# Optimization experiments

Hardware: AMD Instinct MI355X
Metric: run time of the kernel (lower is better)

## Reference

```python
import jax, jax.numpy as jnp
import numpy as np

B, S, D_IN, D_OUT = 4, 2048, 2048, 2048


def setup_inputs() -> dict:
    key = jax.random.key(0)
    k1, k2, k3, k4 = jax.random.split(key, 4)
    x = jax.random.normal(k1, (B, S, D_IN), dtype=jnp.float32)
    scale = 1.0 / np.sqrt(D_IN)
    Wq = jax.random.normal(k2, (D_IN, D_OUT), dtype=jnp.float32) * scale
    Wk = jax.random.normal(k3, (D_IN, D_OUT), dtype=jnp.float32) * scale
    Wv = jax.random.normal(k4, (D_IN, D_OUT), dtype=jnp.float32) * scale
    return {"x": x, "Wq": Wq, "Wk": Wk, "Wv": Wv}


def reference(x, Wq, Wk, Wv):
    # x: [B,S,D_in]; Wq/Wk/Wv: [D_in,D_out]
    q = x @ Wq  # [B,S,D_out]
    k = x @ Wk
    v = x @ Wv
    d_out = q.shape[-1]
    inv_sqrt_d = jnp.asarray(1.0 / np.sqrt(d_out), dtype=x.dtype)
    scores = jnp.einsum('bqd,bkd->bqk', q, k) * inv_sqrt_d  # [B,S,S]
    n = scores.shape[-1]
    causal = jnp.tril(jnp.ones((n, n), dtype=bool))  # True where attending allowed
    scores = jnp.where(causal[None, :, :], scores, jnp.asarray(-jnp.inf, scores.dtype))
    attn = jax.nn.softmax(scores, axis=-1)  # dropout p=0.0 -> identity
    return jnp.einsum('bqk,bkd->bqd', attn, v)  # [B,S,D_out]
```

## Files before the change

### kernel.cpp

```cpp
#include <hip/hip_runtime.h>
#include <cmath>

typedef __bf16 bfx8 __attribute__((ext_vector_type(8)));
typedef float f32x4 __attribute__((ext_vector_type(4)));
typedef unsigned short u16x8 __attribute__((ext_vector_type(8)));

static constexpr int BB = 4, SS = 2048, DD = 2048;

__device__ __forceinline__ unsigned short f2bf(float f) {
  unsigned u = __builtin_bit_cast(unsigned, f);
  u += 0x7fffu + ((u >> 16) & 1u);
  return (unsigned short)(u >> 16);
}

__device__ __forceinline__ void gload_lds16(const void* g, void* l) {
  __builtin_amdgcn_global_load_lds(
      (__attribute__((address_space(1))) unsigned int*)(g),
      (__attribute__((address_space(3))) unsigned int*)(l),
      16, 0, 0);
}

template <int CMODE>
__global__ __launch_bounds__(256) void gemm_bt(
    const unsigned short* __restrict__ A, const unsigned short* __restrict__ B,
    void* __restrict__ Cv, int N, int K,
    long long sA, long long sB, long long sC, float scale)
{
  const int bx = blockIdx.x, by = blockIdx.y, bz = blockIdx.z;
  if (CMODE == 1 && bx > by) return;
  const int t = threadIdx.x;
  const int wave = t >> 6, lane = t & 63;
  const int fr = lane & 15, fk = lane >> 4;
  const int m0 = by << 7, n0 = bx << 7;

  __shared__ __align__(16) char lds[32768];

  const unsigned short* Ab = A + (size_t)bz * sA;
  const unsigned short* Bb = B + (size_t)bz * sB;

  const unsigned short* aSrc[4];
  const unsigned short* bSrc[4];
  int ldsOff[4];
#pragma unroll
  for (int i = 0; i < 4; ++i) {
    int c = i * 256 + t;
    int row = c >> 3;
    int scb = ((c & 7) << 4) ^ ((row & 7) << 4);
    aSrc[i] = Ab + (size_t)(m0 + row) * K + (scb >> 1);
    bSrc[i] = Bb + (size_t)(n0 + row) * K + (scb >> 1);
    ldsOff[i] = i * 4096 + wave * 1024;
  }

  int ktiles = K >> 6;
  if (CMODE == 2) ktiles = min(ktiles, (by + 1) * 2);

  f32x4 acc[4][4] = {};
  const int wr = (wave >> 1) << 6;
  const int wc = (wave & 1) << 6;
  const int sx = (fr & 7) << 4;

  for (int kt = 0; kt < ktiles; ++kt) {
    __syncthreads();
#pragma unroll
    for (int i = 0; i < 4; ++i) {
      gload_lds16(aSrc[i], &lds[ldsOff[i]]);
      gload_lds16(bSrc[i], &lds[16384 + ldsOff[i]]);
      aSrc[i] += 64;
      bSrc[i] += 64;
    }
    __syncthreads();
#pragma unroll
    for (int kk = 0; kk < 2; ++kk) {
      bfx8 af[4], bfv[4];
#pragma unroll
      for (int mi = 0; mi < 4; ++mi) {
        int ar = wr + mi * 16 + fr;
        af[mi] = *(const bfx8*)&lds[ar * 128 + ((kk * 64 + fk * 16) ^ sx)];
      }
#pragma unroll
      for (int ni = 0; ni < 4; ++ni) {
        int br = wc + ni * 16 + fr;
        bfv[ni] = *(const bfx8*)&lds[16384 + br * 128 + ((kk * 64 + fk * 16) ^ sx)];
      }
#pragma unroll
      for (int mi = 0; mi < 4; ++mi)
#pragma unroll
        for (int ni = 0; ni < 4; ++ni)
          acc[mi][ni] = __builtin_amdgcn_mfma_f32_16x16x32_bf16(
              af[mi], bfv[ni], acc[mi][ni], 0, 0, 0);
    }
  }

#pragma unroll
  for (int mi = 0; mi < 4; ++mi) {
#pragma unroll
    for (int ni = 0; ni < 4; ++ni) {
      int r0 = m0 + wr + mi * 16 + fk * 4;
      int cn = n0 + wc + ni * 16 + fr;
      if (CMODE == 0) {
        unsigned short* C = (unsigned short*)Cv + (size_t)bz * sC;
#pragma unroll
        for (int j = 0; j < 4; ++j)
          C[(size_t)(r0 + j) * N + cn] = f2bf(acc[mi][ni][j]);
      } else if (CMODE == 1 || CMODE == 2) {
        float* C = (float*)Cv + (size_t)bz * sC;
#pragma unroll
        for (int j = 0; j < 4; ++j)
          C[(size_t)(r0 + j) * N + cn] = acc[mi][ni][j] * scale;
      } else {
        unsigned short* VT = (unsigned short*)Cv;
        int b = r0 >> 11, s0v = r0 & 2047;
        ushort4 pk;
        pk.x = f2bf(acc[mi][ni][0]);
        pk.y = f2bf(acc[mi][ni][1]);
        pk.z = f2bf(acc[mi][ni][2]);
        pk.w = f2bf(acc[mi][ni][3]);
        *(ushort4*)&VT[(size_t)b * DD * SS + (size_t)cn * SS + s0v] = pk;
      }
    }
  }
}

__global__ __launch_bounds__(256) void cvt_x_kernel(
    const float* __restrict__ x, unsigned short* __restrict__ xb)
{
  size_t i = ((size_t)blockIdx.x * 256 + threadIdx.x) * 8;
  float4 a = *(const float4*)(x + i);
  float4 b = *(const float4*)(x + i + 4);
  u16x8 o = {f2bf(a.x), f2bf(a.y), f2bf(a.z), f2bf(a.w),
             f2bf(b.x), f2bf(b.y), f2bf(b.z), f2bf(b.w)};
  *(u16x8*)(xb + i) = o;
}

__global__ __launch_bounds__(256) void cvt_wT_kernel(
    const float* __restrict__ Wq, const float* __restrict__ Wk,
    const float* __restrict__ Wv, unsigned short* __restrict__ Wt)
{
  const float* W = blockIdx.z == 0 ? Wq : (blockIdx.z == 1 ? Wk : Wv);
  unsigned short* out = Wt + (size_t)blockIdx.z * DD * DD;
  __shared__ unsigned short tile[64][65];
  int k0 = blockIdx.y * 64, n0 = blockIdx.x * 64;
#pragma unroll
  for (int i = 0; i < 16; ++i) {
    int idx = threadIdx.x + i * 256;
    int r = idx >> 6, c = idx & 63;
    tile[r][c] = f2bf(W[(size_t)(k0 + r) * DD + n0 + c]);
  }
  __syncthreads();
#pragma unroll
  for (int i = 0; i < 16; ++i) {
    int idx = threadIdx.x + i * 256;
    int r = idx >> 6, c = idx & 63;
    out[(size_t)(n0 + r) * DD + k0 + c] = tile[c][r];
  }
}

__global__ __launch_bounds__(256) void softmax_causal(
    const float* __restrict__ Sc, unsigned short* __restrict__ P)
{
  const int i = blockIdx.x, b = blockIdx.y, t = threadIdx.x;
  const float* srow = Sc + ((size_t)b * SS + i) * SS;
  unsigned short* prow = P + ((size_t)b * SS + i) * SS;
  const int j0 = t * 8;
  float4 v0 = *(const float4*)(srow + j0);
  float4 v1 = *(const float4*)(srow + j0 + 4);
  float s[8] = {v0.x, v0.y, v0.z, v0.w, v1.x, v1.y, v1.z, v1.w};
  float mx = -INFINITY;
#pragma unroll
  for (int e = 0; e < 8; ++e) {
    if (j0 + e > i) s[e] = -INFINITY;
    mx = fmaxf(mx, s[e]);
  }
#pragma unroll
  for (int off = 32; off; off >>= 1) mx = fmaxf(mx, __shfl_xor(mx, off));
  __shared__ float red[8];
  if ((t & 63) == 0) red[t >> 6] = mx;
  __syncthreads();
  mx = fmaxf(fmaxf(red[0], red[1]), fmaxf(red[2], red[3]));
  float e8[8];
  float sm = 0.f;
#pragma unroll
  for (int e = 0; e < 8; ++e) {
    e8[e] = (j0 + e <= i) ? __expf(s[e] - mx) : 0.f;
    sm += e8[e];
  }
#pragma unroll
  for (int off = 32; off; off >>= 1) sm += __shfl_xor(sm, off);
  if ((t & 63) == 0) red[4 + (t >> 6)] = sm;
  __syncthreads();
  float inv = 1.0f / (red[4] + red[5] + red[6] + red[7]);
  u16x8 o;
#pragma unroll
  for (int e = 0; e < 8; ++e) o[e] = f2bf(e8[e] * inv);
  *(u16x8*)(prow + j0) = o;
}

extern "C" void kernel_launch(void* const* d_in, const int* in_sizes, int n_in,
                              void* d_out, int out_size, void* d_ws, size_t ws_size,
                              hipStream_t stream)
{
  const float* x  = (const float*)d_in[0];
  const float* Wq = (const float*)d_in[1];
  const float* Wk = (const float*)d_in[2];
  const float* Wv = (const float*)d_in[3];
  float* out = (float*)d_out;

  const size_t MR = (size_t)BB * SS;
  unsigned short* xb = (unsigned short*)d_ws;
  unsigned short* Wt = xb + MR * DD;
  unsigned short* qk = Wt + 3ull * DD * DD;
  unsigned short* vt = qk + 2ull * MR * DD;
  float* sc = (float*)(vt + (size_t)BB * DD * SS);
  unsigned short* P = (unsigned short*)(sc + (size_t)BB * SS * SS);

  cvt_x_kernel<<<dim3(8192), 256, 0, stream>>>(x, xb);
  cvt_wT_kernel<<<dim3(32, 32, 3), 256, 0, stream>>>(Wq, Wk, Wv, Wt);

  gemm_bt<0><<<dim3(16, 64, 2), 256, 0, stream>>>(
      xb, Wt, qk, DD, DD, 0, (long long)DD * DD, (long long)(MR * DD), 1.f);
  gemm_bt<3><<<dim3(16, 64, 1), 256, 0, stream>>>(
      xb, Wt + 2ull * DD * DD, vt, DD, DD, 0, 0, 0, 1.f);

  const float iscale = 1.0f / sqrtf((float)DD);
  gemm_bt<1><<<dim3(16, 16, 4), 256, 0, stream>>>(
      qk, qk + MR * DD, sc, SS, DD,
      (long long)(SS * (size_t)DD), (long long)(SS * (size_t)DD),
      (long long)(SS * (size_t)SS), iscale);

  softmax_causal<<<dim3(SS, BB), 256, 0, stream>>>(sc, P);

  gemm_bt<2><<<dim3(16, 16, 4), 256, 0, stream>>>(
      P, vt, out, DD, SS,
      (long long)(SS * (size_t)SS), (long long)(DD * (size_t)SS),
      (long long)(SS * (size_t)DD), 1.f);
}
```

Measured before the change: 556.9 us.

## Use 256x256 double-buffered GEMM tiles with 8 waves and compute V^T via swapped operands

The bf16 GEMM kernel moves from 128x128 tiles with 4 waves to 256x256 tiles with 8 waves. It uses a double-buffered 128KB LDS pipeline: the next K-tile's loads are issued partway through the current tile's MFMA work, and MFMA sections are raised in priority with setprio. The special transposed-store path for V is removed, and V^T is produced by a regular GEMM of Wv^T against x, one batch per z slice. This aims to raise data reuse per LDS load and hide global-load latency. In exchange, the large LDS footprint limits occupancy to one block per CU, and the causal GEMMs now skip work at a coarser tile granularity.

```diff
diff --git a/kernel.cpp b/kernel.cpp
--- a/kernel.cpp
+++ b/kernel.cpp
@@ -21,7 +21,7 @@
 }
 
 template <int CMODE>
-__global__ __launch_bounds__(256) void gemm_bt(
+__global__ __launch_bounds__(512, 2) void gemm_bt(
     const unsigned short* __restrict__ A, const unsigned short* __restrict__ B,
     void* __restrict__ Cv, int N, int K,
     long long sA, long long sB, long long sC, float scale)
@@ -31,91 +31,110 @@
   const int t = threadIdx.x;
   const int wave = t >> 6, lane = t & 63;
   const int fr = lane & 15, fk = lane >> 4;
-  const int m0 = by << 7, n0 = bx << 7;
-
-  __shared__ __align__(16) char lds[32768];
+  const int wr = wave >> 2;
+  const int wc = wave & 3;
+  const int m0 = by << 8, n0 = bx << 8;
+
+  __shared__ __align__(16) char lds[131072];
 
   const unsigned short* Ab = A + (size_t)bz * sA;
   const unsigned short* Bb = B + (size_t)bz * sB;
 
-  const unsigned short* aSrc[4];
-  const unsigned short* bSrc[4];
-  int ldsOff[4];
-#pragma unroll
-  for (int i = 0; i < 4; ++i) {
-    int c = i * 256 + t;
+  const unsigned short* aS[4];
+  const unsigned short* bS[4];
+  int lOff[4];
+#pragma unroll
+  for (int j = 0; j < 4; ++j) {
+    int c = ((j >> 1) << 10) + ((j & 1) << 9) + t;
     int row = c >> 3;
-    int scb = ((c & 7) << 4) ^ ((row & 7) << 4);
-    aSrc[i] = Ab + (size_t)(m0 + row) * K + (scb >> 1);
-    bSrc[i] = Bb + (size_t)(n0 + row) * K + (scb >> 1);
-    ldsOff[i] = i * 4096 + wave * 1024;
+    int sb = ((c & 7) << 4) ^ ((row & 7) << 4);
+    aS[j] = Ab + (size_t)(m0 + row) * K + (sb >> 1);
+    bS[j] = Bb + (size_t)(n0 + row) * K + (sb >> 1);
+    lOff[j] = ((j >> 1) << 14) + ((j & 1) << 13) + (wave << 10);
   }
 
   int ktiles = K >> 6;
-  if (CMODE == 2) ktiles = min(ktiles, (by + 1) * 2);
-
-  f32x4 acc[4][4] = {};
-  const int wr = (wave >> 1) << 6;
-  const int wc = (wave & 1) << 6;
+  if (CMODE == 2) ktiles = min(ktiles, (by + 1) * 4);
+
+  f32x4 acc[8][4] = {};
   const int sx = (fr & 7) << 4;
+  const int aRowB = wr << 7;
+  const int bRowB = wc << 6;
+
+#pragma unroll
+  for (int j = 0; j < 4; ++j) { gload_lds16(aS[j], lds + lOff[j]); aS[j] += 64; }
+#pragma unroll
+  for (int j = 0; j < 4; ++j) { gload_lds16(bS[j], lds + 32768 + lOff[j]); bS[j] += 64; }
+  asm volatile("s_waitcnt vmcnt(0)" ::: "memory");
+  __builtin_amdgcn_s_barrier();
 
   for (int kt = 0; kt < ktiles; ++kt) {
-    __syncthreads();
-#pragma unroll
-    for (int i = 0; i < 4; ++i) {
-      gload_lds16(aSrc[i], &lds[ldsOff[i]]);
-      gload_lds16(bSrc[i], &lds[16384 + ldsOff[i]]);
-      aSrc[i] += 64;
-      bSrc[i] += 64;
+    const int cb = (kt & 1) << 16;
+    const int nb = cb ^ 65536;
+    const bool pf = (kt + 1 < ktiles);
+    const char* la = lds + cb;
+    const char* lb = lds + cb + 32768;
+#pragma unroll
+    for (int q = 0; q < 4; ++q) {
+      const int mb = (q & 1) << 2;
+      const int nbf = (q >> 1) << 1;
+      bfx8 af[4][2], bv[2][2];
+#pragma unroll
+      for (int mi = 0; mi < 4; ++mi) {
+        int row = aRowB + ((mb + mi) << 4) + fr;
+#pragma unroll
+        for (int kk = 0; kk < 2; ++kk)
+          af[mi][kk] = *(const bfx8*)(la + row * 128 + (((kk << 6) + (fk << 4)) ^ sx));
+      }
+#pragma unroll
+      for (int ni = 0; ni < 2; ++ni) {
+        int row = bRowB + ((nbf + ni) << 4) + fr;
+#pragma unroll
+        for (int kk = 0; kk < 2; ++kk)
+          bv[ni][kk] = *(const bfx8*)(lb + row * 128 + (((kk << 6) + (fk << 4)) ^ sx));
+      }
+      if (q == 0 && pf) {
+#pragma unroll
+        for (int j = 0; j < 4; ++j) { gload_lds16(aS[j], lds + nb + lOff[j]); aS[j] += 64; }
+      }
+      if (q == 1 && pf) {
+#pragma unroll
+        for (int j = 0; j < 4; ++j) { gload_lds16(bS[j], lds + nb + 32768 + lOff[j]); bS[j] += 64; }
+      }
+      __builtin_amdgcn_s_barrier();
+      asm volatile("s_waitcnt lgkmcnt(0)" ::: "memory");
+      __builtin_amdgcn_sched_barrier(0);
+      __builtin_amdgcn_s_setprio(1);
+#pragma unroll
+      for (int kk = 0; kk < 2; ++kk)
+#pragma unroll
+        for (int mi = 0; mi < 4; ++mi)
+#pragma unroll
+          for (int ni = 0; ni < 2; ++ni)
+            acc[mb + mi][nbf + ni] = __builtin_amdgcn_mfma_f32_16x16x32_bf16(
+                af[mi][kk], bv[ni][kk], acc[mb + mi][nbf + ni], 0, 0, 0);
+      __builtin_amdgcn_s_setprio(0);
+      if (q == 3) asm volatile("s_waitcnt vmcnt(0)" ::: "memory");
+      __builtin_amdgcn_s_barrier();
     }
-    __syncthreads();
-#pragma unroll
-    for (int kk = 0; kk < 2; ++kk) {
-      bfx8 af[4], bfv[4];
-#pragma unroll
-      for (int mi = 0; mi < 4; ++mi) {
-        int ar = wr + mi * 16 + fr;
-        af[mi] = *(const bfx8*)&lds[ar * 128 + ((kk * 64 + fk * 16) ^ sx)];
-      }
-#pragma unroll
-      for (int ni = 0; ni < 4; ++ni) {
-        int br = wc + ni * 16 + fr;
-        bfv[ni] = *(const bfx8*)&lds[16384 + br * 128 + ((kk * 64 + fk * 16) ^ sx)];
-      }
-#pragma unroll
-      for (int mi = 0; mi < 4; ++mi)
-#pragma unroll
-        for (int ni = 0; ni < 4; ++ni)
-          acc[mi][ni] = __builtin_amdgcn_mfma_f32_16x16x32_bf16(
-              af[mi], bfv[ni], acc[mi][ni], 0, 0, 0);
-    }
-  }
-
-#pragma unroll
-  for (int mi = 0; mi < 4; ++mi) {
-#pragma unroll
-    for (int ni = 0; ni < 4; ++ni) {
-      int r0 = m0 + wr + mi * 16 + fk * 4;
-      int cn = n0 + wc + ni * 16 + fr;
+  }
+
+#pragma unroll
+  for (int mf = 0; mf < 8; ++mf) {
+#pragma unroll
+    for (int nf = 0; nf < 4; ++nf) {
+      int r0 = m0 + (wr << 7) + (mf << 4) + (fk << 2);
+      int cn = n0 + (wc << 6) + (nf << 4) + fr;
       if (CMODE == 0) {
         unsigned short* C = (unsigned short*)Cv + (size_t)bz * sC;
 #pragma unroll
         for (int j = 0; j < 4; ++j)
-          C[(size_t)(r0 + j) * N + cn] = f2bf(acc[mi][ni][j]);
-      } else if (CMODE == 1 || CMODE == 2) {
+          C[(size_t)(r0 + j) * N + cn] = f2bf(acc[mf][nf][j]);
+      } else {
         float* C = (float*)Cv + (size_t)bz * sC;
 #pragma unroll
         for (int j = 0; j < 4; ++j)
-          C[(size_t)(r0 + j) * N + cn] = acc[mi][ni][j] * scale;
-      } else {
-        unsigned short* VT = (unsigned short*)Cv;
-        int b = r0 >> 11, s0v = r0 & 2047;
-        ushort4 pk;
-        pk.x = f2bf(acc[mi][ni][0]);
-        pk.y = f2bf(acc[mi][ni][1]);
-        pk.z = f2bf(acc[mi][ni][2]);
-        pk.w = f2bf(acc[mi][ni][3]);
-        *(ushort4*)&VT[(size_t)b * DD * SS + (size_t)cn * SS + s0v] = pk;
+          C[(size_t)(r0 + j) * N + cn] = acc[mf][nf][j] * scale;
       }
     }
   }
@@ -216,20 +235,21 @@
   cvt_x_kernel<<<dim3(8192), 256, 0, stream>>>(x, xb);
   cvt_wT_kernel<<<dim3(32, 32, 3), 256, 0, stream>>>(Wq, Wk, Wv, Wt);
 
-  gemm_bt<0><<<dim3(16, 64, 2), 256, 0, stream>>>(
+  gemm_bt<0><<<dim3(8, 32, 2), 512, 0, stream>>>(
       xb, Wt, qk, DD, DD, 0, (long long)DD * DD, (long long)(MR * DD), 1.f);
-  gemm_bt<3><<<dim3(16, 64, 1), 256, 0, stream>>>(
-      xb, Wt + 2ull * DD * DD, vt, DD, DD, 0, 0, 0, 1.f);
+  gemm_bt<0><<<dim3(8, 8, 4), 512, 0, stream>>>(
+      Wt + 2ull * DD * DD, xb, vt, SS, DD,
+      0, (long long)(SS * (size_t)DD), (long long)(DD * (size_t)SS), 1.f);
 
   const float iscale = 1.0f / sqrtf((float)DD);
-  gemm_bt<1><<<dim3(16, 16, 4), 256, 0, stream>>>(
+  gemm_bt<1><<<dim3(8, 8, 4), 512, 0, stream>>>(
       qk, qk + MR * DD, sc, SS, DD,
       (long long)(SS * (size_t)DD), (long long)(SS * (size_t)DD),
       (long long)(SS * (size_t)SS), iscale);
 
   softmax_causal<<<dim3(SS, BB), 256, 0, stream>>>(sc, P);
 
-  gemm_bt<2><<<dim3(16, 16, 4), 256, 0, stream>>>(
+  gemm_bt<2><<<dim3(8, 8, 4), 512, 0, stream>>>(
       P, vt, out, DD, SS,
       (long long)(SS * (size_t)SS), (long long)(DD * (size_t)SS),
       (long long)(SS * (size_t)DD), 1.f);
```

Result: faster. 506.9 us (-9.0%).
